# Kernel optimization log

Measured on AMD Instinct MI355X. Metric: run time of the kernel, lower is better.

## Reference

```python
import jax, jax.numpy as jnp
import numpy as np

B, N, PHY, C, HID, FC, L, E = 2, 8192, 2, 64, 64, 128, 3, 524288

def _ln(x, g, b, eps=1e-5):
    mu = jnp.mean(x, axis=-1, keepdims=True)
    var = jnp.mean((x - mu) ** 2, axis=-1, keepdims=True)
    return (x - mu) * jax.lax.rsqrt(var + eps) * g + b

def setup_inputs() -> dict:
    key = jax.random.key(0)
    ks = jax.random.split(key, 24)
    s = 1.0 / np.sqrt(C)
    inp = {
        'x': jax.random.normal(ks[0], (B, N, 5), jnp.float32),
        'edge_index': jax.random.randint(ks[1], (2, E), 0, B * N, jnp.int32),
        'fc0_w': jax.random.normal(ks[2], (C, 4), jnp.float32) * 0.5,
        'fc0_b': jnp.zeros((C,), jnp.float32),
        'ln0_g': jnp.ones((C,), jnp.float32),
        'ln0_b': jnp.zeros((C,), jnp.float32),
        'gg_fc1_w': jax.random.normal(ks[3], (L, HID, C), jnp.float32) * s,
        'gg_fc1_b': jnp.zeros((L, HID), jnp.float32),
        'gg_fc2_w': jax.random.normal(ks[4], (L, C, HID), jnp.float32) * s,
        'gg_fc2_b': jnp.zeros((L, C), jnp.float32),
        'gg_weight': jax.random.uniform(ks[5], (L, HID), jnp.float32) + 0.5,
        'gg_freq': jax.random.normal(ks[6], (L, PHY, HID), jnp.float32) * (2 * np.pi),
        'wc_w': jax.random.normal(ks[7], (L, C, C), jnp.float32) * s,
        'wc_b': jnp.zeros((L, C), jnp.float32),
        'ln_g': jnp.ones((L, C), jnp.float32),
        'ln_b': jnp.zeros((L, C), jnp.float32),
        'fc1_w': jax.random.normal(ks[8], (FC, C), jnp.float32) * s,
        'fc1_b': jnp.zeros((FC,), jnp.float32),
        'fc2_w': jax.random.normal(ks[9], (1, FC), jnp.float32) / np.sqrt(FC),
        'fc2_b': jnp.zeros((1,), jnp.float32),
    }
    return inp

def reference(x, edge_index, fc0_w, fc0_b, ln0_g, ln0_b, gg_fc1_w, gg_fc1_b,
              gg_fc2_w, gg_fc2_b, gg_weight, gg_freq, wc_w, wc_b, ln_g, ln_b,
              fc1_w, fc1_b, fc2_w, fc2_b):
    grid = x[:, :, 2:4]           # (B,N,PHY): columns in_dim-phy_dim .. -1
    gw = x[:, :, 4]               # (B,N) grid_weight
    feat = x[:, :, :4]            # (B,N,in_dim)
    src, dst = edge_index[0], edge_index[1]
    grid_f = grid.reshape(-1, PHY)
    gw_f = gw.reshape(-1)
    vec = grid_f[src] - grid_f[dst]                      # (E,PHY)
    dist2 = jnp.sum(vec * vec, axis=-1, keepdims=True)   # (E,1)
    wgt_src = gw_f[src][:, None]                          # (E,1)

    h = feat @ fc0_w.T + fc0_b                            # (B,N,C)
    h = _ln(h, ln0_g, ln0_b)
    for l in range(L):
        w = gg_weight[l]                                  # (HID,)
        gauss = jnp.sqrt((w / jnp.pi) ** PHY) * jnp.exp(-w * dist2)  # (E,HID)
        fourier = jnp.sin(vec @ gg_freq[l])               # (E,HID)
        morlet = gauss * fourier
        hl = h @ gg_fc1_w[l].T + gg_fc1_b[l]              # (B,N,HID)
        val = morlet * hl.reshape(-1, HID)[src] * wgt_src # (E,HID)
        agg = jax.ops.segment_sum(val, dst, num_segments=B * N)
        x1 = agg.reshape(B, N, HID) @ gg_fc2_w[l].T + gg_fc2_b[l]
        x2 = h @ wc_w[l].T + wc_b[l]                      # pointwise Conv1d
        h = _ln(x1 + x2, ln_g[l], ln_b[l])
        if l != L - 1:
            h = jax.nn.gelu(h, approximate=False)
    h = jax.nn.gelu(h @ fc1_w.T + fc1_b, approximate=False)
    return h @ fc2_w.T + fc2_b                            # (B,N,1)
```

## Files before the change

kernel.cpp:

```cpp
#include <hip/hip_runtime.h>
#include <hip/hip_bf16.h>

#define M_NODES 16384
#define E_EDGES 524288
#define ASTR 68

typedef short short8 __attribute__((ext_vector_type(8)));
typedef float f32x4 __attribute__((ext_vector_type(4)));
typedef unsigned int uint4v __attribute__((ext_vector_type(4)));

#define PK_W1 0
#define PK_WC 12288
#define PK_W2 24576
#define PK_FC1 36864
#define PK_TOTAL 45056

static __device__ __forceinline__ float wredsum(float v) {
#pragma unroll
  for (int o = 32; o > 0; o >>= 1) v += __shfl_xor(v, o, 64);
  return v;
}

static __device__ __forceinline__ float gelu_exact(float x) {
  return 0.5f * x * (1.0f + erff(x * 0.70710678118654752440f));
}

static __device__ __forceinline__ unsigned int bsplit(float x) {
  unsigned int u = __float_as_uint(x);
  unsigned int hb = (u + 0x7FFFu + ((u >> 16) & 1u)) >> 16;
  float hf = __uint_as_float(hb << 16);
  float r = x - hf;
  unsigned int v = __float_as_uint(r);
  unsigned int lb = (v + 0x7FFFu + ((v >> 16) & 1u)) >> 16;
  return (hb & 0xFFFFu) | (lb << 16);
}

struct Frag { short8 hi, lo; };

static __device__ __forceinline__ Frag load_afrag(const unsigned int* a) {
  uint4v u0 = *(const uint4v*)a;
  uint4v u1 = *(const uint4v*)(a + 4);
  Frag f;
#pragma unroll
  for (int j = 0; j < 4; ++j) {
    f.hi[j]     = (short)(u0[j] & 0xFFFFu);
    f.lo[j]     = (short)(u0[j] >> 16);
    f.hi[j + 4] = (short)(u1[j] & 0xFFFFu);
    f.lo[j + 4] = (short)(u1[j] >> 16);
  }
  return f;
}

static __device__ __forceinline__ Frag load_bfrag(const float* __restrict__ w) {
  float4 w0 = *(const float4*)w;
  float4 w1 = *(const float4*)(w + 4);
  float v[8] = {w0.x, w0.y, w0.z, w0.w, w1.x, w1.y, w1.z, w1.w};
  Frag f;
#pragma unroll
  for (int j = 0; j < 8; ++j) {
    unsigned int p = bsplit(v[j]);
    f.hi[j] = (short)(p & 0xFFFFu);
    f.lo[j] = (short)(p >> 16);
  }
  return f;
}

static __device__ __forceinline__ f32x4 mfma3(const Frag& a, const Frag& b, f32x4 c) {
  c = __builtin_amdgcn_mfma_f32_16x16x32_bf16(a.hi, b.hi, c, 0, 0, 0);
  c = __builtin_amdgcn_mfma_f32_16x16x32_bf16(a.lo, b.hi, c, 0, 0, 0);
  c = __builtin_amdgcn_mfma_f32_16x16x32_bf16(a.hi, b.lo, c, 0, 0, 0);
  return c;
}

static __device__ __forceinline__ Frag load_bpk(const short* __restrict__ P, int S, int n, int off) {
  Frag f;
  f.hi = *(const short8*)(P + n * 64 + off);
  f.lo = *(const short8*)(P + S + n * 64 + off);
  return f;
}

static __device__ __forceinline__ float rdlanef(float v, int j) {
  return __int_as_float(__builtin_amdgcn_readlane(__float_as_int(v), j));
}

__global__ __launch_bounds__(256) void k_front(
    const float* __restrict__ x,
    const float* __restrict__ fc0_w, const float* __restrict__ fc0_b,
    const float* __restrict__ ln0_g, const float* __restrict__ ln0_b,
    const float* __restrict__ gg_fc1_w, const float* __restrict__ gg_fc1_b,
    const float* __restrict__ wc_w, const float* __restrict__ wc_b,
    const float* __restrict__ gg_fc2_w, const float* __restrict__ fc1_w,
    const int* __restrict__ ei, int* __restrict__ cnt, short* __restrict__ pk,
    float2* __restrict__ grid2, float* __restrict__ gwf,
    float* __restrict__ hlf, float* __restrict__ x2T)
{
  __shared__ unsigned int A[16 * ASTR];
  const int bid = blockIdx.x;
  const int tid = threadIdx.x;

  if (bid >= 3072) {
    int i = (bid - 3072) * 256 + tid;
    float v = (i < PK_WC)  ? gg_fc1_w[i]
            : (i < PK_W2)  ? wc_w[i - PK_WC]
            : (i < PK_FC1) ? gg_fc2_w[i - PK_W2]
                           : fc1_w[i - PK_FC1];
    int mb, sz;
    if (i < PK_FC1) { mb = i & ~4095; sz = 4096; } else { mb = PK_FC1; sz = 8192; }
    int k = i - mb;
    unsigned int p = bsplit(v);
    pk[2 * mb + k]      = (short)(p & 0xFFFFu);
    pk[2 * mb + sz + k] = (short)(p >> 16);
    return;
  }
  if (bid >= 1024) {
    int e = (bid - 1024) * 256 + tid;
    atomicAdd(&cnt[ei[E_EDGES + e]], 1);
    return;
  }

  const int lane = tid & 63, w = tid >> 6;
  const int tilebase = bid * 16;

  float fw0 = fc0_w[lane * 4 + 0], fw1 = fc0_w[lane * 4 + 1];
  float fw2v = fc0_w[lane * 4 + 2], fw3 = fc0_w[lane * 4 + 3];
  float fb = fc0_b[lane], g0 = ln0_g[lane], bb0 = ln0_b[lane];

#pragma unroll
  for (int i = 0; i < 4; ++i) {
    int node = tilebase + 4 * w + i;
    float xv0 = x[node * 5 + 0], xv1 = x[node * 5 + 1], xv2 = x[node * 5 + 2];
    float xv3 = x[node * 5 + 3], xv4 = x[node * 5 + 4];
    float acc = fb + xv0 * fw0 + xv1 * fw1 + xv2 * fw2v + xv3 * fw3;
    float mean = wredsum(acc) * (1.0f / 64.0f);
    float d = acc - mean;
    float var = wredsum(d * d) * (1.0f / 64.0f);
    float hv = d * rsqrtf(var + 1e-5f) * g0 + bb0;
    A[(4 * w + i) * ASTR + lane] = bsplit(hv);
    if (lane == 0) { grid2[node] = make_float2(xv2, xv3); gwf[node] = xv4; }
  }
  __syncthreads();

  const int c = lane & 15, q = lane >> 4;
  const int n = 16 * w + c;

  {
    Frag a0 = load_afrag(A + c * ASTR + 8 * q);
    Frag a1 = load_afrag(A + c * ASTR + 32 + 8 * q);
    Frag b0 = load_bfrag(gg_fc1_w + n * 64 + 8 * q);
    Frag b1 = load_bfrag(gg_fc1_w + n * 64 + 32 + 8 * q);
    f32x4 acc = {0.f, 0.f, 0.f, 0.f};
    acc = mfma3(a0, b0, acc);
    acc = mfma3(a1, b1, acc);
    float b1v = gg_fc1_b[n];
#pragma unroll
    for (int r = 0; r < 4; ++r) {
      float gwr = x[(tilebase + 4 * q + r) * 5 + 4];
      hlf[(tilebase + 4 * q + r) * 64 + n] = (acc[r] + b1v) * gwr;
    }

    Frag c0 = load_bfrag(wc_w + n * 64 + 8 * q);
    Frag c1 = load_bfrag(wc_w + n * 64 + 32 + 8 * q);
    f32x4 ac2 = {0.f, 0.f, 0.f, 0.f};
    ac2 = mfma3(a0, c0, ac2);
    ac2 = mfma3(a1, c1, ac2);
    float wcbv = wc_b[n];
    *(float4*)(x2T + n * M_NODES + tilebase + 4 * q) =
        make_float4(ac2[0] + wcbv, ac2[1] + wcbv, ac2[2] + wcbv, ac2[3] + wcbv);
  }
}

__global__ __launch_bounds__(1024) void k_scan(const int* __restrict__ cnt,
                                               int* __restrict__ row_start,
                                               int* __restrict__ cursor,
                                               int* __restrict__ esrc,
                                               float2* __restrict__ evw)
{
  const int PER = M_NODES / 1024;
  const int t = threadIdx.x;
  const int base = t * PER;
  int local[PER];
  int s = 0;
#pragma unroll
  for (int k = 0; k < PER; ++k) { local[k] = cnt[base + k]; s += local[k]; }

  __shared__ int part[1024];
  part[t] = s;
  __syncthreads();
  for (int off = 1; off < 1024; off <<= 1) {
    int v = (t >= off) ? part[t - off] : 0;
    __syncthreads();
    part[t] += v;
    __syncthreads();
  }
  int run = part[t] - s;
#pragma unroll
  for (int k = 0; k < PER; ++k) {
    row_start[base + k] = run;
    cursor[base + k] = run;
    run += local[k];
  }
  if (t == 1023) row_start[M_NODES] = run;
  if (t == 0) { esrc[E_EDGES] = 0; evw[E_EDGES] = make_float2(0.f, 0.f); }
}

__global__ __launch_bounds__(256) void k_scatter(
    const int* __restrict__ ei, const float2* __restrict__ grid2,
    int* __restrict__ cursor,
    int* __restrict__ esrc, float2* __restrict__ evw)
{
  int e = blockIdx.x * 256 + threadIdx.x;
  if (e < E_EDGES) {
    int s = ei[e];
    int dd = ei[E_EDGES + e];
    int pos = atomicAdd(&cursor[dd], 1);
    float2 gs = grid2[s], gd = grid2[dd];
    esrc[pos] = s;
    evw[pos] = make_float2(gs.x - gd.x, gs.y - gd.y);
  }
}

#define EDGE_PHASE()                                                          \
  const float wv = gw[lane];                                                  \
  const float nwl2 = -wv * 1.44269504088896340736f;                           \
  const float lc = log2f(wv * 0.31830988618379067154f);                       \
  const float f0s = freq[lane] * 0.15915494309189533577f;                     \
  const float f1s = freq[64 + lane] * 0.15915494309189533577f;                \
  const float* __restrict__ hrow = hlf_in + lane;                             \
  for (int nn = 0; nn < 4; ++nn) {                                            \
    const int node = tilebase + 4 * w + nn;                                   \
    const int beg = row_start[node];                                          \
    const int end = row_start[node + 1];                                      \
    float acc = 0.f;                                                          \
    for (int cb = beg; cb < end; cb += 64) {                                  \
      const int cnc = min(64, end - cb);                                      \
      const int idx = (lane < cnc) ? (cb + lane) : E_EDGES;                   \
      const int src_l = esrc[idx];                                            \
      const float2 v_l = evw[idx];                                            \
      const float d2_l = __builtin_fmaf(v_l.x, v_l.x, v_l.y * v_l.y);         \
      float HA[8], HB[8];                                                     \
      auto g8 = [&](float* H, int g) {                                        \
        _Pragma("unroll")                                                     \
        for (int u = 0; u < 8; ++u) {                                         \
          int ss = __builtin_amdgcn_readlane(src_l, 8 * g + u);               \
          H[u] = hrow[(size_t)ss * 64];                                       \
        }                                                                     \
      };                                                                      \
      auto c8 = [&](const float* H, int g) {                                  \
        _Pragma("unroll")                                                     \
        for (int u = 0; u < 8; ++u) {                                         \
          int j = 8 * g + u;                                                  \
          float svx = rdlanef(v_l.x, j);                                      \
          float svy = rdlanef(v_l.y, j);                                      \
          float sd2 = rdlanef(d2_l, j);                                       \
          float ga = __builtin_amdgcn_exp2f(__builtin_fmaf(nwl2, sd2, lc));   \
          float rv = __builtin_fmaf(svx, f0s, svy * f1s);                     \
          float fo = __builtin_amdgcn_sinf(__builtin_amdgcn_fractf(rv));      \
          acc = __builtin_fmaf(ga * fo, H[u], acc);                           \
        }                                                                     \
      };                                                                      \
      const int Gp = (cnc + 7) >> 3;                                          \
      g8(HA, 0);                                                              \
      int g = 0;                                                              \
      for (; g + 2 < Gp; g += 2) {                                            \
        g8(HB, g + 1);                                                        \
        c8(HA, g);                                                            \
        g8(HA, g + 2);                                                        \
        c8(HB, g + 1);                                                        \
      }                                                                       \
      if (g + 1 < Gp) {                                                       \
        g8(HB, g + 1);                                                        \
        c8(HA, g);                                                            \
        c8(HB, g + 1);                                                        \
      } else {                                                                \
        c8(HA, g);                                                            \
      }                                                                       \
    }                                                                         \
    A[(4 * w + nn) * ASTR + lane] = bsplit(acc);                              \
  }

__global__ __launch_bounds__(256) void k_layer_mid(
    const int* __restrict__ esrc, const float2* __restrict__ evw,
    const int* __restrict__ row_start,
    const float* __restrict__ hlf_in, const float* __restrict__ gwf,
    const float* __restrict__ gw, const float* __restrict__ freq,
    const short* __restrict__ pw2, const float* __restrict__ b2,
    const float* __restrict__ lng, const float* __restrict__ lnb,
    const short* __restrict__ pnw1, const float* __restrict__ nb1,
    const short* __restrict__ pnwc, const float* __restrict__ nwcb,
    float* __restrict__ hlf_out, float* __restrict__ x2T)
{
  __shared__ unsigned int A[16 * ASTR];
  __shared__ float PS[4][16], PQ[4][16];
  const int tid = threadIdx.x, lane = tid & 63, w = tid >> 6;
  const int tilebase = blockIdx.x * 16;
  const int c = lane & 15, q = lane >> 4;
  const int n = 16 * w + c;

  float4 x2v = *(const float4*)(x2T + n * M_NODES + tilebase + 4 * q);
  float4 gw4 = *(const float4*)(gwf + tilebase + 4 * q);
  float lg = lng[n], lb = lnb[n], vb = b2[n];
  float b1v = nb1[n], wcbv = nwcb[n];

  EDGE_PHASE()

  Frag wb0 = load_bpk(pw2, 4096, n, 8 * q);
  Frag wb1 = load_bpk(pw2, 4096, n, 32 + 8 * q);
  Frag n10 = load_bpk(pnw1, 4096, n, 8 * q);
  Frag n11 = load_bpk(pnw1, 4096, n, 32 + 8 * q);
  Frag nc0 = load_bpk(pnwc, 4096, n, 8 * q);
  Frag nc1 = load_bpk(pnwc, 4096, n, 32 + 8 * q);
  __syncthreads();

  Frag a0 = load_afrag(A + c * ASTR + 8 * q);
  Frag a1 = load_afrag(A + c * ASTR + 32 + 8 * q);
  f32x4 acc = {0.f, 0.f, 0.f, 0.f};
  acc = mfma3(a0, wb0, acc);
  acc = mfma3(a1, wb1, acc);

  float S[4];
#pragma unroll
  for (int r = 0; r < 4; ++r) S[r] = acc[r] + vb + x2v[r];

#pragma unroll
  for (int r = 0; r < 4; ++r) {
    float s1 = S[r], s2 = S[r] * S[r];
#pragma unroll
    for (int m = 1; m < 16; m <<= 1) {
      s1 += __shfl_xor(s1, m, 64);
      s2 += __shfl_xor(s2, m, 64);
    }
    if (c == 0) { PS[w][4 * q + r] = s1; PQ[w][4 * q + r] = s2; }
  }
  __syncthreads();

#pragma unroll
  for (int r = 0; r < 4; ++r) {
    int row = 4 * q + r;
    float sum = PS[0][row] + PS[1][row] + PS[2][row] + PS[3][row];
    float sq  = PQ[0][row] + PQ[1][row] + PQ[2][row] + PQ[3][row];
    float mean = sum * (1.0f / 64.0f);
    float var = sq * (1.0f / 64.0f) - mean * mean;
    float hv = (S[r] - mean) * rsqrtf(var + 1e-5f) * lg + lb;
    hv = gelu_exact(hv);
    A[row * ASTR + n] = bsplit(hv);
  }
  __syncthreads();

  Frag h0 = load_afrag(A + c * ASTR + 8 * q);
  Frag h1 = load_afrag(A + c * ASTR + 32 + 8 * q);

  f32x4 hh = {0.f, 0.f, 0.f, 0.f};
  hh = mfma3(h0, n10, hh);
  hh = mfma3(h1, n11, hh);
#pragma unroll
  for (int r = 0; r < 4; ++r)
    hlf_out[(tilebase + 4 * q + r) * 64 + n] = (hh[r] + b1v) * gw4[r];

  f32x4 hx = {0.f, 0.f, 0.f, 0.f};
  hx = mfma3(h0, nc0, hx);
  hx = mfma3(h1, nc1, hx);
  *(float4*)(x2T + n * M_NODES + tilebase + 4 * q) =
      make_float4(hx[0] + wcbv, hx[1] + wcbv, hx[2] + wcbv, hx[3] + wcbv);
}

__global__ __launch_bounds__(256) void k_layer_last(
    const int* __restrict__ esrc, const float2* __restrict__ evw,
    const int* __restrict__ row_start,
    const float* __restrict__ hlf_in,
    const float* __restrict__ gw, const float* __restrict__ freq,
    const short* __restrict__ pw2, const float* __restrict__ b2,
    const float* __restrict__ lng, const float* __restrict__ lnb,
    const float* __restrict__ x2T,
    const short* __restrict__ pfc1, const float* __restrict__ fc1b,
    const float* __restrict__ fw2, const float* __restrict__ fb2,
    float* __restrict__ out)
{
  __shared__ unsigned int A[16 * ASTR];
  __shared__ float PS[4][16], PQ[4][16];
  const int tid = threadIdx.x, lane = tid & 63, w = tid >> 6;
  const int tilebase = blockIdx.x * 16;
  const int c = lane & 15, q = lane >> 4;
  const int n = 16 * w + c;

  float4 x2v = *(const float4*)(x2T + n * M_NODES + tilebase + 4 * q);
  float lg = lng[n], lb = lnb[n], vb = b2[n];

  EDGE_PHASE()

  Frag wb0 = load_bpk(pw2, 4096, n, 8 * q);
  Frag wb1 = load_bpk(pw2, 4096, n, 32 + 8 * q);
  __syncthreads();

  Frag a0 = load_afrag(A + c * ASTR + 8 * q);
  Frag a1 = load_afrag(A + c * ASTR + 32 + 8 * q);
  f32x4 acc = {0.f, 0.f, 0.f, 0.f};
  acc = mfma3(a0, wb0, acc);
  acc = mfma3(a1, wb1, acc);

  float S[4];
#pragma unroll
  for (int r = 0; r < 4; ++r) S[r] = acc[r] + vb + x2v[r];

#pragma unroll
  for (int r = 0; r < 4; ++r) {
    float s1 = S[r], s2 = S[r] * S[r];
#pragma unroll
    for (int m = 1; m < 16; m <<= 1) {
      s1 += __shfl_xor(s1, m, 64);
      s2 += __shfl_xor(s2, m, 64);
    }
    if (c == 0) { PS[w][4 * q + r] = s1; PQ[w][4 * q + r] = s2; }
  }
  __syncthreads();

#pragma unroll
  for (int r = 0; r < 4; ++r) {
    int row = 4 * q + r;
    float sum = PS[0][row] + PS[1][row] + PS[2][row] + PS[3][row];
    float sq  = PQ[0][row] + PQ[1][row] + PQ[2][row] + PQ[3][row];
    float mean = sum * (1.0f / 64.0f);
    float var = sq * (1.0f / 64.0f) - mean * mean;
    float hv = (S[r] - mean) * rsqrtf(var + 1e-5f) * lg + lb;
    A[row * ASTR + n] = bsplit(hv);
  }
  __syncthreads();

  Frag ha0 = load_afrag(A + c * ASTR + 8 * q);
  Frag ha1 = load_afrag(A + c * ASTR + 32 + 8 * q);
  float p[4] = {0.f, 0.f, 0.f, 0.f};
#pragma unroll
  for (int half = 0; half < 2; ++half) {
    int row = 32 * w + 16 * half + c;
    Frag b0 = load_bpk(pfc1, 8192, row, 8 * q);
    Frag b1 = load_bpk(pfc1, 8192, row, 32 + 8 * q);
    f32x4 a = {0.f, 0.f, 0.f, 0.f};
    a = mfma3(ha0, b0, a);
    a = mfma3(ha1, b1, a);
    float fbv = fc1b[row], fwv = fw2[row];
#pragma unroll
    for (int r = 0; r < 4; ++r) p[r] += gelu_exact(a[r] + fbv) * fwv;
  }
#pragma unroll
  for (int r = 0; r < 4; ++r) {
    float s = p[r];
#pragma unroll
    for (int m = 1; m < 16; m <<= 1) s += __shfl_xor(s, m, 64);
    if (c == 0) PS[w][4 * q + r] = s;
  }
  __syncthreads();
  if (tid < 16)
    out[tilebase + tid] = PS[0][tid] + PS[1][tid] + PS[2][tid] + PS[3][tid] + fb2[0];
}

extern "C" void kernel_launch(void* const* d_in, const int* in_sizes, int n_in,
                              void* d_out, int out_size, void* d_ws, size_t ws_size,
                              hipStream_t stream) {
  const float* x     = (const float*)d_in[0];
  const int* ei      = (const int*)d_in[1];
  const float* fc0_w = (const float*)d_in[2];
  const float* fc0_b = (const float*)d_in[3];
  const float* ln0_g = (const float*)d_in[4];
  const float* ln0_b = (const float*)d_in[5];
  const float* gg_fc1_w = (const float*)d_in[6];
  const float* gg_fc1_b = (const float*)d_in[7];
  const float* gg_fc2_w = (const float*)d_in[8];
  const float* gg_fc2_b = (const float*)d_in[9];
  const float* gg_weight = (const float*)d_in[10];
  const float* gg_freq   = (const float*)d_in[11];
  const float* wc_w = (const float*)d_in[12];
  const float* wc_b = (const float*)d_in[13];
  const float* ln_g = (const float*)d_in[14];
  const float* ln_b = (const float*)d_in[15];
  const float* fc1_w = (const float*)d_in[16];
  const float* fc1_b = (const float*)d_in[17];
  const float* fc2_w = (const float*)d_in[18];
  const float* fc2_b = (const float*)d_in[19];

  char* ws = (char*)d_ws;
  size_t off = 0;
  auto alloc = [&](size_t bytes) -> void* {
    void* p = ws + off;
    off = (off + bytes + 255) & ~(size_t)255;
    return p;
  };
  float2* grid2 = (float2*)alloc((size_t)M_NODES * 8);
  float*  gwf   = (float*)alloc((size_t)M_NODES * 4);
  float*  hlf_a = (float*)alloc((size_t)M_NODES * 64 * 4);
  float*  hlf_b = (float*)alloc((size_t)M_NODES * 64 * 4);
  float*  x2T   = (float*)alloc((size_t)M_NODES * 64 * 4);
  int*    cnt   = (int*)alloc((size_t)M_NODES * 4);
  int*    cursor= (int*)alloc((size_t)M_NODES * 4);
  int*    row_st= (int*)alloc((size_t)(M_NODES + 1) * 4);
  int*    esrc  = (int*)alloc((size_t)(E_EDGES + 1) * 4);
  float2* evw   = (float2*)alloc((size_t)(E_EDGES + 1) * 8);
  short*  pk    = (short*)alloc((size_t)PK_TOTAL * 2 * 2);
  (void)ws_size; (void)in_sizes; (void)n_in; (void)out_size;

  hipMemsetAsync(cnt, 0, (size_t)M_NODES * 4, stream);

  k_front<<<3248, 256, 0, stream>>>(x, fc0_w, fc0_b, ln0_g, ln0_b,
                                    gg_fc1_w, gg_fc1_b, wc_w, wc_b,
                                    gg_fc2_w, fc1_w,
                                    ei, cnt, pk, grid2, gwf, hlf_a, x2T);
  k_scan<<<1, 1024, 0, stream>>>(cnt, row_st, cursor, esrc, evw);
  k_scatter<<<E_EDGES / 256, 256, 0, stream>>>(ei, grid2, cursor, esrc, evw);

  k_layer_mid<<<M_NODES / 16, 256, 0, stream>>>(
      esrc, evw, row_st, hlf_a, gwf, gg_weight + 0 * 64, gg_freq + 0 * 128,
      pk + 2 * (PK_W2 + 0 * 4096), gg_fc2_b + 0 * 64,
      ln_g + 0 * 64, ln_b + 0 * 64,
      pk + 2 * (PK_W1 + 1 * 4096), gg_fc1_b + 1 * 64,
      pk + 2 * (PK_WC + 1 * 4096), wc_b + 1 * 64,
      hlf_b, x2T);
  k_layer_mid<<<M_NODES / 16, 256, 0, stream>>>(
      esrc, evw, row_st, hlf_b, gwf, gg_weight + 1 * 64, gg_freq + 1 * 128,
      pk + 2 * (PK_W2 + 1 * 4096), gg_fc2_b + 1 * 64,
      ln_g + 1 * 64, ln_b + 1 * 64,
      pk + 2 * (PK_W1 + 2 * 4096), gg_fc1_b + 2 * 64,
      pk + 2 * (PK_WC + 2 * 4096), wc_b + 2 * 64,
      hlf_a, x2T);
  k_layer_last<<<M_NODES / 16, 256, 0, stream>>>(
      esrc, evw, row_st, hlf_a, gg_weight + 2 * 64, gg_freq + 2 * 128,
      pk + 2 * (PK_W2 + 2 * 4096), gg_fc2_b + 2 * 64,
      ln_g + 2 * 64, ln_b + 2 * 64,
      x2T,
      pk + 2 * PK_FC1, fc1_b, fc2_w, fc2_b,
      (float*)d_out);
}
```

Measured before the change: 251.9 us.

## Pack edge records into float4 with precomputed dist2 and prefetch chunks

Replaces the separate esrc and evw edge arrays with one 16-byte record holding dx, dy, dist2 and the source index, so each edge needs one vector load. dist2 is computed once in the scatter kernel instead of in each layer. The edge phase now issues the first-chunk loads for all four nodes up front and prefetches the next 64-edge chunk while the current one is processed, to hide load latency. Edge storage grows from 12 to 16 bytes per edge, and the preloaded records raise register pressure.

```diff
diff --git a/kernel.cpp b/kernel.cpp
--- a/kernel.cpp
+++ b/kernel.cpp
@@ -172,8 +172,7 @@
 __global__ __launch_bounds__(1024) void k_scan(const int* __restrict__ cnt,
                                                int* __restrict__ row_start,
                                                int* __restrict__ cursor,
-                                               int* __restrict__ esrc,
-                                               float2* __restrict__ evw)
+                                               float4* __restrict__ erec)
 {
   const int PER = M_NODES / 1024;
   const int t = threadIdx.x;
@@ -200,13 +199,12 @@
     run += local[k];
   }
   if (t == 1023) row_start[M_NODES] = run;
-  if (t == 0) { esrc[E_EDGES] = 0; evw[E_EDGES] = make_float2(0.f, 0.f); }
+  if (t == 0) erec[E_EDGES] = make_float4(0.f, 0.f, 0.f, 0.f);
 }
 
 __global__ __launch_bounds__(256) void k_scatter(
     const int* __restrict__ ei, const float2* __restrict__ grid2,
-    int* __restrict__ cursor,
-    int* __restrict__ esrc, float2* __restrict__ evw)
+    int* __restrict__ cursor, float4* __restrict__ erec)
 {
   int e = blockIdx.x * 256 + threadIdx.x;
   if (e < E_EDGES) {
@@ -214,8 +212,9 @@
     int dd = ei[E_EDGES + e];
     int pos = atomicAdd(&cursor[dd], 1);
     float2 gs = grid2[s], gd = grid2[dd];
-    esrc[pos] = s;
-    evw[pos] = make_float2(gs.x - gd.x, gs.y - gd.y);
+    float dx = gs.x - gd.x, dy = gs.y - gd.y;
+    float d2 = __builtin_fmaf(dx, dx, dy * dy);
+    erec[pos] = make_float4(dx, dy, d2, __int_as_float(s));
   }
 }
 
@@ -226,61 +225,77 @@
   const float f0s = freq[lane] * 0.15915494309189533577f;                     \
   const float f1s = freq[64 + lane] * 0.15915494309189533577f;                \
   const float* __restrict__ hrow = hlf_in + lane;                             \
-  for (int nn = 0; nn < 4; ++nn) {                                            \
-    const int node = tilebase + 4 * w + nn;                                   \
-    const int beg = row_start[node];                                          \
-    const int end = row_start[node + 1];                                      \
-    float acc = 0.f;                                                          \
-    for (int cb = beg; cb < end; cb += 64) {                                  \
-      const int cnc = min(64, end - cb);                                      \
-      const int idx = (lane < cnc) ? (cb + lane) : E_EDGES;                   \
-      const int src_l = esrc[idx];                                            \
-      const float2 v_l = evw[idx];                                            \
-      const float d2_l = __builtin_fmaf(v_l.x, v_l.x, v_l.y * v_l.y);         \
-      float HA[8], HB[8];                                                     \
-      auto g8 = [&](float* H, int g) {                                        \
-        _Pragma("unroll")                                                     \
-        for (int u = 0; u < 8; ++u) {                                         \
-          int ss = __builtin_amdgcn_readlane(src_l, 8 * g + u);               \
-          H[u] = hrow[(size_t)ss * 64];                                       \
+  {                                                                           \
+    int rs[5];                                                                \
+    _Pragma("unroll")                                                         \
+    for (int nn = 0; nn < 5; ++nn) rs[nn] = row_start[tilebase + 4 * w + nn]; \
+    float4 C[4];                                                              \
+    _Pragma("unroll")                                                         \
+    for (int nn = 0; nn < 4; ++nn) {                                          \
+      int idx = (rs[nn] + lane < rs[nn + 1]) ? (rs[nn] + lane) : E_EDGES;     \
+      C[nn] = erec[idx];                                                      \
+    }                                                                         \
+    _Pragma("unroll")                                                         \
+    for (int nn = 0; nn < 4; ++nn) {                                          \
+      const int end = rs[nn + 1];                                             \
+      float acc = 0.f;                                                        \
+      float4 cur = C[nn];                                                     \
+      int cb = rs[nn];                                                        \
+      while (true) {                                                          \
+        const int cnc = min(64, end - cb);                                    \
+        const bool more = (cb + 64 < end);                                    \
+        float4 nxt;                                                           \
+        if (more) {                                                           \
+          int idx = (cb + 64 + lane < end) ? (cb + 64 + lane) : E_EDGES;      \
+          nxt = erec[idx];                                                    \
         }                                                                     \
-      };                                                                      \
-      auto c8 = [&](const float* H, int g) {                                  \
-        _Pragma("unroll")                                                     \
-        for (int u = 0; u < 8; ++u) {                                         \
-          int j = 8 * g + u;                                                  \
-          float svx = rdlanef(v_l.x, j);                                      \
-          float svy = rdlanef(v_l.y, j);                                      \
-          float sd2 = rdlanef(d2_l, j);                                       \
-          float ga = __builtin_amdgcn_exp2f(__builtin_fmaf(nwl2, sd2, lc));   \
-          float rv = __builtin_fmaf(svx, f0s, svy * f1s);                     \
-          float fo = __builtin_amdgcn_sinf(__builtin_amdgcn_fractf(rv));      \
-          acc = __builtin_fmaf(ga * fo, H[u], acc);                           \
+        float HA[8], HB[8];                                                   \
+        auto g8 = [&](float* H, int g) {                                      \
+          _Pragma("unroll")                                                   \
+          for (int u = 0; u < 8; ++u) {                                       \
+            int ss = __builtin_amdgcn_readlane(__float_as_int(cur.w),         \
+                                               8 * g + u);                    \
+            H[u] = hrow[(size_t)ss * 64];                                     \
+          }                                                                   \
+        };                                                                    \
+        auto c8 = [&](const float* H, int g) {                                \
+          _Pragma("unroll")                                                   \
+          for (int u = 0; u < 8; ++u) {                                       \
+            int j = 8 * g + u;                                                \
+            float svx = rdlanef(cur.x, j);                                    \
+            float svy = rdlanef(cur.y, j);                                    \
+            float sd2 = rdlanef(cur.z, j);                                    \
+            float ga = __builtin_amdgcn_exp2f(__builtin_fmaf(nwl2, sd2, lc)); \
+            float rv = __builtin_fmaf(svx, f0s, svy * f1s);                   \
+            float fo = __builtin_amdgcn_sinf(__builtin_amdgcn_fractf(rv));    \
+            acc = __builtin_fmaf(ga * fo, H[u], acc);                         \
+          }                                                                   \
+        };                                                                    \
+        const int Gp = (cnc + 7) >> 3;                                        \
+        g8(HA, 0);                                                            \
+        int g = 0;                                                            \
+        for (; g + 2 < Gp; g += 2) {                                          \
+          g8(HB, g + 1);                                                      \
+          c8(HA, g);                                                          \
+          g8(HA, g + 2);                                                      \
+          c8(HB, g + 1);                                                      \
         }                                                                     \
-      };                                                                      \
-      const int Gp = (cnc + 7) >> 3;                                          \
-      g8(HA, 0);                                                              \
-      int g = 0;                                                              \
-      for (; g + 2 < Gp; g += 2) {                                            \
-        g8(HB, g + 1);                                                        \
-        c8(HA, g);                                                            \
-        g8(HA, g + 2);                                                        \
-        c8(HB, g + 1);                                                        \
+        if (g + 1 < Gp) {                                                     \
+          g8(HB, g + 1);                                                      \
+          c8(HA, g);                                                          \
+          c8(HB, g + 1);                                                      \
+        } else {                                                              \
+          c8(HA, g);                                                          \
+        }                                                                     \
+        if (!more) break;                                                     \
+        cur = nxt; cb += 64;                                                  \
       }                                                                       \
-      if (g + 1 < Gp) {                                                       \
-        g8(HB, g + 1);                                                        \
-        c8(HA, g);                                                            \
-        c8(HB, g + 1);                                                        \
-      } else {                                                                \
-        c8(HA, g);                                                            \
-      }                                                                       \
+      A[(4 * w + nn) * ASTR + lane] = bsplit(acc);                            \
     }                                                                         \
-    A[(4 * w + nn) * ASTR + lane] = bsplit(acc);                              \
   }
 
 __global__ __launch_bounds__(256) void k_layer_mid(
-    const int* __restrict__ esrc, const float2* __restrict__ evw,
-    const int* __restrict__ row_start,
+    const float4* __restrict__ erec, const int* __restrict__ row_start,
     const float* __restrict__ hlf_in, const float* __restrict__ gwf,
     const float* __restrict__ gw, const float* __restrict__ freq,
     const short* __restrict__ pw2, const float* __restrict__ b2,
@@ -364,8 +379,7 @@
 }
 
 __global__ __launch_bounds__(256) void k_layer_last(
-    const int* __restrict__ esrc, const float2* __restrict__ evw,
-    const int* __restrict__ row_start,
+    const float4* __restrict__ erec, const int* __restrict__ row_start,
     const float* __restrict__ hlf_in,
     const float* __restrict__ gw, const float* __restrict__ freq,
     const short* __restrict__ pw2, const float* __restrict__ b2,
@@ -491,8 +505,7 @@
   int*    cnt   = (int*)alloc((size_t)M_NODES * 4);
   int*    cursor= (int*)alloc((size_t)M_NODES * 4);
   int*    row_st= (int*)alloc((size_t)(M_NODES + 1) * 4);
-  int*    esrc  = (int*)alloc((size_t)(E_EDGES + 1) * 4);
-  float2* evw   = (float2*)alloc((size_t)(E_EDGES + 1) * 8);
+  float4* erec  = (float4*)alloc((size_t)(E_EDGES + 1) * 16);
   short*  pk    = (short*)alloc((size_t)PK_TOTAL * 2 * 2);
   (void)ws_size; (void)in_sizes; (void)n_in; (void)out_size;
 
@@ -502,25 +515,25 @@
                                     gg_fc1_w, gg_fc1_b, wc_w, wc_b,
                                     gg_fc2_w, fc1_w,
                                     ei, cnt, pk, grid2, gwf, hlf_a, x2T);
-  k_scan<<<1, 1024, 0, stream>>>(cnt, row_st, cursor, esrc, evw);
-  k_scatter<<<E_EDGES / 256, 256, 0, stream>>>(ei, grid2, cursor, esrc, evw);
+  k_scan<<<1, 1024, 0, stream>>>(cnt, row_st, cursor, erec);
+  k_scatter<<<E_EDGES / 256, 256, 0, stream>>>(ei, grid2, cursor, erec);
 
   k_layer_mid<<<M_NODES / 16, 256, 0, stream>>>(
-      esrc, evw, row_st, hlf_a, gwf, gg_weight + 0 * 64, gg_freq + 0 * 128,
+      erec, row_st, hlf_a, gwf, gg_weight + 0 * 64, gg_freq + 0 * 128,
       pk + 2 * (PK_W2 + 0 * 4096), gg_fc2_b + 0 * 64,
       ln_g + 0 * 64, ln_b + 0 * 64,
       pk + 2 * (PK_W1 + 1 * 4096), gg_fc1_b + 1 * 64,
       pk + 2 * (PK_WC + 1 * 4096), wc_b + 1 * 64,
       hlf_b, x2T);
   k_layer_mid<<<M_NODES / 16, 256, 0, stream>>>(
-      esrc, evw, row_st, hlf_b, gwf, gg_weight + 1 * 64, gg_freq + 1 * 128,
+      erec, row_st, hlf_b, gwf, gg_weight + 1 * 64, gg_freq + 1 * 128,
       pk + 2 * (PK_W2 + 1 * 4096), gg_fc2_b + 1 * 64,
       ln_g + 1 * 64, ln_b + 1 * 64,
       pk + 2 * (PK_W1 + 2 * 4096), gg_fc1_b + 2 * 64,
       pk + 2 * (PK_WC + 2 * 4096), wc_b + 2 * 64,
       hlf_a, x2T);
   k_layer_last<<<M_NODES / 16, 256, 0, stream>>>(
-      esrc, evw, row_st, hlf_a, gg_weight + 2 * 64, gg_freq + 2 * 128,
+      erec, row_st, hlf_a, gg_weight + 2 * 64, gg_freq + 2 * 128,
       pk + 2 * (PK_W2 + 2 * 4096), gg_fc2_b + 2 * 64,
       ln_g + 2 * 64, ln_b + 2 * 64,
       x2T,
```

New measurement: 251.9 us. About the same (+0.0%).
